# Optimization experiments

Measured on AMD Instinct MI355X. Metric: run time of the kernel, lower is better.

## Reference

```python
import jax, jax.numpy as jnp
import numpy as np

N_STEPS = 50          # t_span=(0,1), step_size=0.02
STEP_SIZE = 0.02
A_SCALE = 0.1         # keep linear ODE stable over 50 Euler steps


def setup_inputs() -> dict:
    key = jax.random.key(0)
    ks = jax.random.split(key, 5)
    B, D, H, O = 1048576, 64, 256, 16
    x = jax.random.normal(ks[0], (B, D), dtype=jnp.float32)
    A = jax.random.normal(ks[1], (D, D), dtype=jnp.float32) * A_SCALE
    W1 = jax.random.normal(ks[2], (D, H), dtype=jnp.float32) * (1.0 / np.sqrt(D))
    b1 = jnp.zeros((H,), dtype=jnp.float32)
    W2 = jax.random.normal(ks[3], (H, O), dtype=jnp.float32) * (1.0 / np.sqrt(H))
    b2 = jnp.zeros((O,), dtype=jnp.float32)
    return {"x": x, "A": A, "W1": W1, "b1": b1, "W2": W2, "b2": b2}


def reference(x, A, W1, b1, W2, b2):
    # explicit Euler on dz/dt = z @ A, 50 steps from t=0 to t=1
    def step(z, _):
        z = z + STEP_SIZE * (z @ A)
        return z, None
    zT, _ = jax.lax.scan(step, x, None, length=N_STEPS)
    # Q head: Linear -> Tanh -> Linear
    h = jnp.tanh(zT @ W1 + b1)
    return h @ W2 + b2
```

## Files before the change

kernel.cpp:

```cpp
#include <hip/hip_runtime.h>

typedef float f32x4 __attribute__((ext_vector_type(4)));
typedef __bf16 bf16x8 __attribute__((ext_vector_type(8)));
typedef _Float16 f16x2 __attribute__((ext_vector_type(2)));
typedef _Float16 f16x8 __attribute__((ext_vector_type(8)));

#define LDT 68

__device__ __forceinline__ unsigned short bf16_bits(float f) {
    return __builtin_bit_cast(unsigned short, (__bf16)f);
}
__device__ __forceinline__ unsigned short f16_bits(float f) {
    return __builtin_bit_cast(unsigned short, (_Float16)f);
}

__device__ __forceinline__ unsigned tanh2_pk(float a, float b) {
    f16x2 v = __builtin_bit_cast(f16x2, __builtin_amdgcn_cvt_pkrtz(a, b));
    f16x2 x2 = v * v;
    f16x2 x4 = x2 * x2;
    const f16x2 c945 = {(_Float16)945.f, (_Float16)945.f};
    const f16x2 c105 = {(_Float16)105.f, (_Float16)105.f};
    const f16x2 c420 = {(_Float16)420.f, (_Float16)420.f};
    const f16x2 c15  = {(_Float16)15.f,  (_Float16)15.f};
    const f16x2 one  = {(_Float16)1.f,   (_Float16)1.f};
    f16x2 num = v * (c945 + c105 * x2 + x4);
    f16x2 den = c945 + c420 * x2 + c15 * x4;
    unsigned r0u = 0x77807780u - __builtin_bit_cast(unsigned, den);
    f16x2 r = __builtin_bit_cast(f16x2, r0u);
    r = r + r * (one - den * r);
    r = r + r * (one - den * r);
    return __builtin_bit_cast(unsigned, num * r);
}
__device__ __forceinline__ float clamp4(float v) {
    return __builtin_amdgcn_fmed3f(v, -4.0f, 4.0f);
}

__global__ __launch_bounds__(256) void ode_pre1(
        const float* __restrict__ A, const float* __restrict__ W2,
        unsigned short* __restrict__ ws) {
    __shared__ float Ts[64 * LDT];
    __shared__ float Za[64 * LDT];
    __shared__ float ZaT[64 * LDT];
    __shared__ float Zb[64 * LDT];
    __shared__ float ZbT[64 * LDT];
    const int t = threadIdx.x;

    for (int i = t; i < 4096; i += 256) {
        int r = i >> 6, c = i & 63;
        float v = 0.02f * A[i] + ((r == c) ? 1.0f : 0.0f);
        Ts[r * LDT + c] = v;
        Za[r * LDT + c] = v;
        ZaT[c * LDT + r] = v;
    }
    __syncthreads();

    const int r0 = (t >> 4) * 4;
    const int c0 = (t & 15) * 4;
    auto mm = [&](const float* XT, const float* Y, float* Z, float* ZT) {
        float ac[4][4];
        #pragma unroll
        for (int i = 0; i < 4; i++)
            #pragma unroll
            for (int j = 0; j < 4; j++) ac[i][j] = 0.0f;
        #pragma unroll 8
        for (int k = 0; k < 64; k++) {
            float4 a = *(const float4*)(XT + k * LDT + r0);
            float4 b = *(const float4*)(Y + k * LDT + c0);
            ac[0][0] = fmaf(a.x, b.x, ac[0][0]); ac[0][1] = fmaf(a.x, b.y, ac[0][1]);
            ac[0][2] = fmaf(a.x, b.z, ac[0][2]); ac[0][3] = fmaf(a.x, b.w, ac[0][3]);
            ac[1][0] = fmaf(a.y, b.x, ac[1][0]); ac[1][1] = fmaf(a.y, b.y, ac[1][1]);
            ac[1][2] = fmaf(a.y, b.z, ac[1][2]); ac[1][3] = fmaf(a.y, b.w, ac[1][3]);
            ac[2][0] = fmaf(a.z, b.x, ac[2][0]); ac[2][1] = fmaf(a.z, b.y, ac[2][1]);
            ac[2][2] = fmaf(a.z, b.z, ac[2][2]); ac[2][3] = fmaf(a.z, b.w, ac[2][3]);
            ac[3][0] = fmaf(a.w, b.x, ac[3][0]); ac[3][1] = fmaf(a.w, b.y, ac[3][1]);
            ac[3][2] = fmaf(a.w, b.z, ac[3][2]); ac[3][3] = fmaf(a.w, b.w, ac[3][3]);
        }
        #pragma unroll
        for (int i = 0; i < 4; i++)
            *(float4*)(Z + (r0 + i) * LDT + c0) =
                make_float4(ac[i][0], ac[i][1], ac[i][2], ac[i][3]);
        #pragma unroll
        for (int j = 0; j < 4; j++)
            *(float4*)(ZT + (c0 + j) * LDT + r0) =
                make_float4(ac[0][j], ac[1][j], ac[2][j], ac[3][j]);
        __syncthreads();
    };
    mm(ZaT, Za, Zb, ZbT);
    mm(ZbT, Ts, Za, ZaT);
    mm(ZaT, Za, Zb, ZbT);
    mm(ZbT, Zb, Za, ZaT);
    mm(ZaT, Za, Zb, ZbT);
    mm(ZbT, Ts, Za, ZaT);
    mm(ZaT, Za, Zb, ZbT);

    float* gM = (float*)(ws + 20480);
    for (int i = t; i < 4096; i += 256)
        gM[i] = Zb[(i >> 6) * LDT + (i & 63)];

    #pragma unroll
    for (int e = 0; e < 16; e++) {
        int f = t * 16 + e;
        int tt = f >> 9, l = (f >> 3) & 63, j = f & 7;
        int qq = l >> 4, cc = l & 15;
        int n = 16 * (2 * tt + (j >> 2)) + 4 * qq + (j & 3);
        ws[16384 + f] = f16_bits(W2[n * 16 + cc]);
    }
}

__global__ __launch_bounds__(256) void ode_pre2(
        const float* __restrict__ W1, unsigned short* __restrict__ ws) {
    const float* M = (const float*)(ws + 20480);
    const int k = blockIdx.x;
    const int col = threadIdx.x;
    const float* mrow = M + k * 64;
    float acc = 0.0f;
    #pragma unroll 8
    for (int d = 0; d < 64; d++)
        acc = fmaf(mrow[d], W1[d * 256 + col], acc);
    const int ntg = col >> 4, cc = col & 15;
    const int kt = k >> 5, qq = (k >> 3) & 3, jj = k & 7;
    ws[((ntg * 2 + kt) * 64 + qq * 16 + cc) * 8 + jj] = bf16_bits(acc);
}

__global__ __launch_bounds__(512, 4) void ode_main(
        const float* __restrict__ x, const unsigned short* __restrict__ wsfrag,
        const float* __restrict__ b1, const float* __restrict__ b2,
        float* __restrict__ out, int B) {
    __shared__ unsigned short w1f[16384];
    __shared__ unsigned short w2f[4096];
    __shared__ float b1s[256];
    const int t = threadIdx.x;
    const int wid = t >> 6, lane = t & 63;
    const int q = lane >> 4, c = lane & 15;
    const long rowbase = (long)blockIdx.x * 256 + wid * 32;

    float4 xraw[8];
    #pragma unroll
    for (int s = 0; s < 2; s++) {
        long row = rowbase + 16 * s + c;
        if (row >= B) row = B - 1;
        const float* xp = x + row * 64 + q * 8;
        xraw[s * 4 + 0] = *(const float4*)(xp);
        xraw[s * 4 + 1] = *(const float4*)(xp + 4);
        xraw[s * 4 + 2] = *(const float4*)(xp + 32);
        xraw[s * 4 + 3] = *(const float4*)(xp + 36);
    }

    {
        const uint4* src = (const uint4*)wsfrag;
        uint4* d1 = (uint4*)w1f;
        #pragma unroll
        for (int i = 0; i < 4; i++) d1[t + 512 * i] = src[t + 512 * i];
        ((uint4*)w2f)[t] = src[2048 + t];
        if (t < 64) ((float4*)b1s)[t] = ((const float4*)b1)[t];
    }
    __syncthreads();

    bf16x8 xb[2][2];
    #pragma unroll
    for (int s = 0; s < 2; s++)
        #pragma unroll
        for (int kt = 0; kt < 2; kt++) {
            float4 u0 = xraw[s * 4 + kt * 2];
            float4 u1 = xraw[s * 4 + kt * 2 + 1];
            bf16x8 cv;
            cv[0] = (__bf16)u0.x; cv[1] = (__bf16)u0.y;
            cv[2] = (__bf16)u0.z; cv[3] = (__bf16)u0.w;
            cv[4] = (__bf16)u1.x; cv[5] = (__bf16)u1.y;
            cv[6] = (__bf16)u1.z; cv[7] = (__bf16)u1.w;
            xb[s][kt] = cv;
        }

    f32x4 oacc[2] = {{0, 0, 0, 0}, {0, 0, 0, 0}};
    #pragma unroll 1
    for (int Q = 0; Q < 4; Q++) {
        f32x4 acc[2][4];
        #pragma unroll
        for (int m = 0; m < 4; m++) {
            float4 bb = *(const float4*)(b1s + 16 * (4 * Q + m) + 4 * q);
            f32x4 bv = {bb.x, bb.y, bb.z, bb.w};
            acc[0][m] = bv;
            acc[1][m] = bv;
        }
        #pragma unroll
        for (int kt = 0; kt < 2; kt++) {
            #pragma unroll
            for (int m = 0; m < 4; m++) {
                uint4 wraw = *(const uint4*)(w1f + (((4 * Q + m) * 2 + kt) * 64 + lane) * 8);
                bf16x8 wv = __builtin_bit_cast(bf16x8, wraw);
                acc[0][m] = __builtin_amdgcn_mfma_f32_16x16x32_bf16(wv, xb[0][kt], acc[0][m], 0, 0, 0);
                acc[1][m] = __builtin_amdgcn_mfma_f32_16x16x32_bf16(wv, xb[1][kt], acc[1][m], 0, 0, 0);
            }
        }
        #pragma unroll
        for (int p = 0; p < 2; p++) {
            const int tt = 2 * Q + p;
            uint4 w2r = *(const uint4*)(w2f + (tt * 64 + lane) * 8);
            f16x8 w2v = __builtin_bit_cast(f16x8, w2r);
            #pragma unroll
            for (int s = 0; s < 2; s++) {
                const f32x4 ae = acc[s][2 * p];
                const f32x4 ao = acc[s][2 * p + 1];
                uint4 pr;
                pr.x = tanh2_pk(clamp4(ae[0]), clamp4(ae[1]));
                pr.y = tanh2_pk(clamp4(ae[2]), clamp4(ae[3]));
                pr.z = tanh2_pk(clamp4(ao[0]), clamp4(ao[1]));
                pr.w = tanh2_pk(clamp4(ao[2]), clamp4(ao[3]));
                f16x8 pa = __builtin_bit_cast(f16x8, pr);
                oacc[s] = __builtin_amdgcn_mfma_f32_16x16x32_f16(w2v, pa, oacc[s], 0, 0, 0);
            }
        }
    }
    const float4 b2v4 = *(const float4*)(b2 + 4 * q);
    #pragma unroll
    for (int s = 0; s < 2; s++) {
        long row = rowbase + 16 * s + c;
        if (row < B)
            *(float4*)(out + row * 16 + 4 * q) =
                make_float4(oacc[s][0] + b2v4.x, oacc[s][1] + b2v4.y,
                            oacc[s][2] + b2v4.z, oacc[s][3] + b2v4.w);
    }
}

extern "C" void kernel_launch(void* const* d_in, const int* in_sizes, int n_in,
                              void* d_out, int out_size, void* d_ws, size_t ws_size,
                              hipStream_t stream) {
    const float* x  = (const float*)d_in[0];
    const float* A  = (const float*)d_in[1];
    const float* W1 = (const float*)d_in[2];
    const float* b1 = (const float*)d_in[3];
    const float* W2 = (const float*)d_in[4];
    const float* b2 = (const float*)d_in[5];
    float* out = (float*)d_out;
    unsigned short* ws = (unsigned short*)d_ws;

    const int B = in_sizes[0] / 64;

    ode_pre1<<<1, 256, 0, stream>>>(A, W2, ws);
    ode_pre2<<<64, 256, 0, stream>>>(W1, ws);
    const int grid = (B + 255) / 256;
    ode_main<<<grid, 512, 0, stream>>>(x, ws, b1, b2, out, B);
}
```

Before: 126.7 us.

## Process two 256-row tiles per block to amortize weight staging

Each block now handles two consecutive 256-row tiles in a loop, so the shared-memory copy of the W1/W2 fragments is paid once per 512 rows and the grid is halved. The b1 bias is no longer staged in shared memory; it is read from global memory and added after the MFMA chain, which now starts from zero accumulators. The second tile's x loads are issued only after the first tile's compute, so there is less overlap across blocks, and the global bias reads add load traffic inside the inner loop.

```diff
diff --git a/kernel.cpp b/kernel.cpp
--- a/kernel.cpp
+++ b/kernel.cpp
@@ -6,6 +6,7 @@
 typedef _Float16 f16x8 __attribute__((ext_vector_type(8)));
 
 #define LDT 68
+#define NITER 2
 
 __device__ __forceinline__ unsigned short bf16_bits(float f) {
     return __builtin_bit_cast(unsigned short, (__bf16)f);
@@ -128,16 +129,15 @@
         float* __restrict__ out, int B) {
     __shared__ unsigned short w1f[16384];
     __shared__ unsigned short w2f[4096];
-    __shared__ float b1s[256];
     const int t = threadIdx.x;
     const int wid = t >> 6, lane = t & 63;
     const int q = lane >> 4, c = lane & 15;
-    const long rowbase = (long)blockIdx.x * 256 + wid * 32;
+    const long blockbase = (long)blockIdx.x * (256L * NITER);
 
     float4 xraw[8];
     #pragma unroll
     for (int s = 0; s < 2; s++) {
-        long row = rowbase + 16 * s + c;
+        long row = blockbase + wid * 32 + 16 * s + c;
         if (row >= B) row = B - 1;
         const float* xp = x + row * 64 + q * 8;
         xraw[s * 4 + 0] = *(const float4*)(xp);
@@ -152,73 +152,90 @@
         #pragma unroll
         for (int i = 0; i < 4; i++) d1[t + 512 * i] = src[t + 512 * i];
         ((uint4*)w2f)[t] = src[2048 + t];
-        if (t < 64) ((float4*)b1s)[t] = ((const float4*)b1)[t];
     }
     __syncthreads();
 
-    bf16x8 xb[2][2];
-    #pragma unroll
-    for (int s = 0; s < 2; s++)
-        #pragma unroll
-        for (int kt = 0; kt < 2; kt++) {
-            float4 u0 = xraw[s * 4 + kt * 2];
-            float4 u1 = xraw[s * 4 + kt * 2 + 1];
-            bf16x8 cv;
-            cv[0] = (__bf16)u0.x; cv[1] = (__bf16)u0.y;
-            cv[2] = (__bf16)u0.z; cv[3] = (__bf16)u0.w;
-            cv[4] = (__bf16)u1.x; cv[5] = (__bf16)u1.y;
-            cv[6] = (__bf16)u1.z; cv[7] = (__bf16)u1.w;
-            xb[s][kt] = cv;
-        }
-
-    f32x4 oacc[2] = {{0, 0, 0, 0}, {0, 0, 0, 0}};
+    const float4 b2v4 = *(const float4*)(b2 + 4 * q);
+    const f32x4 zero4 = {0.0f, 0.0f, 0.0f, 0.0f};
+
     #pragma unroll 1
-    for (int Q = 0; Q < 4; Q++) {
-        f32x4 acc[2][4];
-        #pragma unroll
-        for (int m = 0; m < 4; m++) {
-            float4 bb = *(const float4*)(b1s + 16 * (4 * Q + m) + 4 * q);
-            f32x4 bv = {bb.x, bb.y, bb.z, bb.w};
-            acc[0][m] = bv;
-            acc[1][m] = bv;
-        }
-        #pragma unroll
-        for (int kt = 0; kt < 2; kt++) {
+    for (int it = 0; it < NITER; ++it) {
+        const long rowbase = blockbase + it * 256 + wid * 32;
+        if (it > 0) {
+            #pragma unroll
+            for (int s = 0; s < 2; s++) {
+                long row = rowbase + 16 * s + c;
+                if (row >= B) row = B - 1;
+                const float* xp = x + row * 64 + q * 8;
+                xraw[s * 4 + 0] = *(const float4*)(xp);
+                xraw[s * 4 + 1] = *(const float4*)(xp + 4);
+                xraw[s * 4 + 2] = *(const float4*)(xp + 32);
+                xraw[s * 4 + 3] = *(const float4*)(xp + 36);
+            }
+        }
+        bf16x8 xb[2][2];
+        #pragma unroll
+        for (int s = 0; s < 2; s++)
+            #pragma unroll
+            for (int kt = 0; kt < 2; kt++) {
+                float4 u0 = xraw[s * 4 + kt * 2];
+                float4 u1 = xraw[s * 4 + kt * 2 + 1];
+                bf16x8 cv;
+                cv[0] = (__bf16)u0.x; cv[1] = (__bf16)u0.y;
+                cv[2] = (__bf16)u0.z; cv[3] = (__bf16)u0.w;
+                cv[4] = (__bf16)u1.x; cv[5] = (__bf16)u1.y;
+                cv[6] = (__bf16)u1.z; cv[7] = (__bf16)u1.w;
+                xb[s][kt] = cv;
+            }
+
+        f32x4 oacc[2] = {{0, 0, 0, 0}, {0, 0, 0, 0}};
+        #pragma unroll 1
+        for (int Q = 0; Q < 4; Q++) {
+            float4 bb[4];
+            #pragma unroll
+            for (int m = 0; m < 4; m++)
+                bb[m] = *(const float4*)(b1 + 16 * (4 * Q + m) + 4 * q);
+            f32x4 acc[2][4];
             #pragma unroll
             for (int m = 0; m < 4; m++) {
-                uint4 wraw = *(const uint4*)(w1f + (((4 * Q + m) * 2 + kt) * 64 + lane) * 8);
-                bf16x8 wv = __builtin_bit_cast(bf16x8, wraw);
-                acc[0][m] = __builtin_amdgcn_mfma_f32_16x16x32_bf16(wv, xb[0][kt], acc[0][m], 0, 0, 0);
-                acc[1][m] = __builtin_amdgcn_mfma_f32_16x16x32_bf16(wv, xb[1][kt], acc[1][m], 0, 0, 0);
-            }
-        }
-        #pragma unroll
-        for (int p = 0; p < 2; p++) {
-            const int tt = 2 * Q + p;
-            uint4 w2r = *(const uint4*)(w2f + (tt * 64 + lane) * 8);
-            f16x8 w2v = __builtin_bit_cast(f16x8, w2r);
-            #pragma unroll
-            for (int s = 0; s < 2; s++) {
-                const f32x4 ae = acc[s][2 * p];
-                const f32x4 ao = acc[s][2 * p + 1];
-                uint4 pr;
-                pr.x = tanh2_pk(clamp4(ae[0]), clamp4(ae[1]));
-                pr.y = tanh2_pk(clamp4(ae[2]), clamp4(ae[3]));
-                pr.z = tanh2_pk(clamp4(ao[0]), clamp4(ao[1]));
-                pr.w = tanh2_pk(clamp4(ao[2]), clamp4(ao[3]));
-                f16x8 pa = __builtin_bit_cast(f16x8, pr);
-                oacc[s] = __builtin_amdgcn_mfma_f32_16x16x32_f16(w2v, pa, oacc[s], 0, 0, 0);
-            }
-        }
-    }
-    const float4 b2v4 = *(const float4*)(b2 + 4 * q);
-    #pragma unroll
-    for (int s = 0; s < 2; s++) {
-        long row = rowbase + 16 * s + c;
-        if (row < B)
-            *(float4*)(out + row * 16 + 4 * q) =
-                make_float4(oacc[s][0] + b2v4.x, oacc[s][1] + b2v4.y,
-                            oacc[s][2] + b2v4.z, oacc[s][3] + b2v4.w);
+                uint4 wr0 = *(const uint4*)(w1f + (((4 * Q + m) * 2 + 0) * 64 + lane) * 8);
+                uint4 wr1 = *(const uint4*)(w1f + (((4 * Q + m) * 2 + 1) * 64 + lane) * 8);
+                bf16x8 wv0 = __builtin_bit_cast(bf16x8, wr0);
+                bf16x8 wv1 = __builtin_bit_cast(bf16x8, wr1);
+                #pragma unroll
+                for (int s = 0; s < 2; s++) {
+                    f32x4 a = __builtin_amdgcn_mfma_f32_16x16x32_bf16(wv0, xb[s][0], zero4, 0, 0, 0);
+                    acc[s][m] = __builtin_amdgcn_mfma_f32_16x16x32_bf16(wv1, xb[s][1], a, 0, 0, 0);
+                }
+            }
+            #pragma unroll
+            for (int p = 0; p < 2; p++) {
+                const int tt = 2 * Q + p;
+                uint4 w2r = *(const uint4*)(w2f + (tt * 64 + lane) * 8);
+                f16x8 w2v = __builtin_bit_cast(f16x8, w2r);
+                const float4 be = bb[2 * p], bo = bb[2 * p + 1];
+                #pragma unroll
+                for (int s = 0; s < 2; s++) {
+                    const f32x4 ae = acc[s][2 * p];
+                    const f32x4 ao = acc[s][2 * p + 1];
+                    uint4 pr;
+                    pr.x = tanh2_pk(clamp4(ae[0] + be.x), clamp4(ae[1] + be.y));
+                    pr.y = tanh2_pk(clamp4(ae[2] + be.z), clamp4(ae[3] + be.w));
+                    pr.z = tanh2_pk(clamp4(ao[0] + bo.x), clamp4(ao[1] + bo.y));
+                    pr.w = tanh2_pk(clamp4(ao[2] + bo.z), clamp4(ao[3] + bo.w));
+                    f16x8 pa = __builtin_bit_cast(f16x8, pr);
+                    oacc[s] = __builtin_amdgcn_mfma_f32_16x16x32_f16(w2v, pa, oacc[s], 0, 0, 0);
+                }
+            }
+        }
+        #pragma unroll
+        for (int s = 0; s < 2; s++) {
+            long row = rowbase + 16 * s + c;
+            if (row < B)
+                *(float4*)(out + row * 16 + 4 * q) =
+                    make_float4(oacc[s][0] + b2v4.x, oacc[s][1] + b2v4.y,
+                                oacc[s][2] + b2v4.z, oacc[s][3] + b2v4.w);
+        }
     }
 }
 
@@ -238,6 +255,7 @@
 
     ode_pre1<<<1, 256, 0, stream>>>(A, W2, ws);
     ode_pre2<<<64, 256, 0, stream>>>(W1, ws);
-    const int grid = (B + 255) / 256;
+    const long rows_per_block = 256L * NITER;
+    const int grid = (int)((B + rows_per_block - 1) / rows_per_block);
     ode_main<<<grid, 512, 0, stream>>>(x, ws, b1, b2, out, B);
 }
```

Result: slower. 158.3 us (+24.9%).
